# Performance work log

Hardware: AMD Instinct MI355X
Metric: run time of the kernel (lower is better)

The kernel has to match this reference:

```python
import jax, jax.numpy as jnp
import numpy as np


def _dct1d_last(x, W_r, W_i):
    """DCT-II along last axis via the even/odd-reorder + FFT trick, ortho norm.

    x: [..., N] real. W_r/W_i: [1, N] rows = cos/sin(-k*pi/(2N)).
    """
    N = x.shape[-1]
    # v = [x[0], x[2], ...] ++ [x[N-1], x[N-3], ..., x[1]]  (torch index/inverted_index)
    v = jnp.concatenate([x[..., 0::2], x[..., 1::2][..., ::-1]], axis=-1)
    Vc = jnp.fft.fft(v, axis=-1)  # complex64
    V = Vc.real * W_r - Vc.imag * W_i  # [..., N]
    # ortho normalization: V[0] /= sqrt(N)*2 ; V[1:] /= sqrt(N/2)*2 ; then V *= 2
    s0 = 1.0 / (np.sqrt(N) * 2.0)
    s1 = 1.0 / (np.sqrt(N / 2.0) * 2.0)
    scale = jnp.concatenate([jnp.full((1,), s0, x.dtype), jnp.full((N - 1,), s1, x.dtype)])
    return 2.0 * V * scale


def setup_inputs() -> dict:
    key = jax.random.key(0)
    H, W = 512, 512
    x = jax.random.normal(key, (32, 3, H, W), dtype=jnp.float32)
    kw = -jnp.arange(W, dtype=jnp.float32)[None, :] * np.pi / (2 * W)
    kh = -jnp.arange(H, dtype=jnp.float32)[None, :] * np.pi / (2 * H)
    return {
        "x": x,
        "W_r_weight": jnp.cos(kw), "W_i_weight": jnp.sin(kw),
        "W_r_height": jnp.cos(kh), "W_i_height": jnp.sin(kh),
    }


def reference(x, W_r_weight, W_i_weight, W_r_height, W_i_height):
    # DCT along width (last axis)
    V = _dct1d_last(x, W_r_weight, W_i_weight)
    # transpose last two dims, DCT along height, transpose back
    V = jnp.swapaxes(V, -1, -2)
    V = _dct1d_last(V, W_r_height, W_i_height)
    return jnp.swapaxes(V, -1, -2)
```

## Files before the change

kernel.cpp:

```cpp
#include <hip/hip_runtime.h>
#include <math.h>

#define NN 512

typedef __attribute__((ext_vector_type(8))) short bf16x8;
typedef __attribute__((ext_vector_type(4))) float f32x4;
typedef __attribute__((ext_vector_type(4))) unsigned int u32x4;

__device__ inline unsigned short f2bf(float f) {
    unsigned u = __builtin_bit_cast(unsigned, f);
    u += 0x7fffu + ((u >> 16) & 1u);
    return (unsigned short)(u >> 16);
}
__device__ inline float bf2f(unsigned short h) {
    unsigned u = ((unsigned)h) << 16;
    return __builtin_bit_cast(float, u);
}
__device__ inline unsigned cvtpk_bf16(float lo, float hi) {
    unsigned r;
    asm("v_cvt_pk_bf16_f32 %0, %1, %2" : "=v"(r) : "v"(lo), "v"(hi));
    return r;
}

__global__ __launch_bounds__(256) void fill_dct_half(unsigned short* __restrict__ Ce,
                                                     unsigned short* __restrict__ Co) {
    int idx = blockIdx.x * 256 + threadIdx.x;
    int par = idx >> 16;
    int kk = (idx >> 8) & 255;
    int n = idx & 255;
    int k = 2 * kk + par;
    int m = ((2 * n + 1) * k) & 2047;
    float ang = (float)m * 3.0679615757712823e-3f;
    float s = (k == 0) ? 0.04419417382415922f : 0.0625f;
    unsigned short v = f2bf(s * cosf(ang));
    if (par) Co[kk * 256 + n] = v; else Ce[kk * 256 + n] = v;
}

#define GLB(p) ((const __attribute__((address_space(1))) unsigned int*)(const void*)(p))
#define LDS(p) ((__attribute__((address_space(3))) unsigned int*)(p))

template <int PASS>
__global__ __launch_bounds__(256, 3) void gemm_dct(const void* __restrict__ Ap,
                                                   const unsigned short* __restrict__ Ce,
                                                   const unsigned short* __restrict__ Cop,
                                                   void* __restrict__ Outp,
                                                   size_t strideIn, size_t strideOut) {
    const int nwg = (int)gridDim.x;
    const int cpx = nwg >> 3;
    const int bid = (int)blockIdx.x;
    const int nid = (bid & 7) * cpx + (bid >> 3);
    const int bx = nid & 3;
    const int by = (nid >> 2) & 3;
    const int bz = nid >> 4;

    __shared__ unsigned short sm[24576];
    unsigned short* As = sm;
    unsigned short* Bs = sm + 12288;

    const int t = threadIdx.x;
    const int lane = t & 63;
    const int wave = t >> 6;
    const int wr = wave >> 1, wc = wave & 1;
    const int lr = lane & 15;
    const int kgx = ((lane >> 4) * 8) ^ (((lr >> 1) & 3) << 3);

    const int srow = t >> 2;
    const int sslot = t & 3;
    const int scol = (sslot ^ ((srow >> 1) & 3)) * 8;

    const int frow = t >> 1;
    const int fhalf = t & 1;
    const int fs0 = fhalf * 2;
    const int fxw = (frow >> 1) & 3;
    const int fslot0 = (fs0 ^ fxw) * 8;
    const int fslot1 = ((fs0 + 1) ^ fxw) * 8;

    const float* Xf = nullptr;
    const unsigned short* Tp = nullptr;
    const unsigned short* Gmat;
    int grow0, sgn, row0, col0;
    if constexpr (PASS == 1) {
        Xf = (const float*)Ap + (size_t)bz * strideIn;
        row0 = by * 128;
        col0 = bx * 128;
        Gmat = (bx < 2) ? Ce : Cop; grow0 = (bx & 1) * 128; sgn = (bx >= 2);
    } else {
        Tp = (const unsigned short*)Ap + (size_t)bz * strideIn;
        col0 = bx * 128;
        row0 = 0;
        Gmat = (by < 2) ? Ce : Cop; grow0 = (by & 1) * 128; sgn = (by >= 2);
    }
    const float sgnf = sgn ? -1.0f : 1.0f;

    f32x4 acc[4][4] = {};

    f32x4 rf[4], rm[4];
    bf16x8 gf[2], gm[2];

    auto stageG = [&](unsigned short* dst, int buf, int k0) {
        __builtin_amdgcn_global_load_lds(GLB(Gmat + (size_t)(grow0 + srow) * 256 + k0 + scol),
                                         LDS(&dst[buf * 4096 + srow * 32 + sslot * 8]), 16, 0, 0);
        __builtin_amdgcn_global_load_lds(GLB(Gmat + (size_t)(grow0 + 64 + srow) * 256 + k0 + scol),
                                         LDS(&dst[buf * 4096 + (64 + srow) * 32 + sslot * 8]), 16, 0, 0);
    };
    auto loadRaw1 = [&](int k0) {
        const float* bfp = Xf + (size_t)(row0 + frow) * NN + k0 + fhalf * 16;
        const float* bmp = Xf + (size_t)(row0 + frow) * NN + (496 - k0 - fhalf * 16);
#pragma unroll
        for (int q = 0; q < 4; ++q) {
            rf[q] = *reinterpret_cast<const f32x4*>(bfp + 4 * q);
            rm[q] = *reinterpret_cast<const f32x4*>(bmp + 4 * q);
        }
    };
    auto combineWrite1 = [&](int buf) {
        unsigned p[8];
#pragma unroll
        for (int q = 0; q < 8; ++q) {
            const int j0 = 2 * q, j1 = 2 * q + 1;
            const int r0 = 15 - j0, r1 = 15 - j1;
            float s0 = fmaf(sgnf, rm[r0 >> 2][r0 & 3], rf[j0 >> 2][j0 & 3]);
            float s1 = fmaf(sgnf, rm[r1 >> 2][r1 & 3], rf[j1 >> 2][j1 & 3]);
            p[q] = cvtpk_bf16(s0, s1);
        }
        u32x4 w0 = {p[0], p[1], p[2], p[3]};
        u32x4 w1 = {p[4], p[5], p[6], p[7]};
        *reinterpret_cast<u32x4*>(&As[buf * 4096 + frow * 32 + fslot0]) = w0;
        *reinterpret_cast<u32x4*>(&As[buf * 4096 + frow * 32 + fslot1]) = w1;
    };
    auto loadRaw2 = [&](int k0) {
        const unsigned short* bfp = Tp + (size_t)(col0 + frow) * NN + k0 + fhalf * 16;
        const unsigned short* bmp = Tp + (size_t)(col0 + frow) * NN + (496 - k0 - fhalf * 16);
        gf[0] = *reinterpret_cast<const bf16x8*>(bfp);
        gf[1] = *reinterpret_cast<const bf16x8*>(bfp + 8);
        gm[0] = *reinterpret_cast<const bf16x8*>(bmp);
        gm[1] = *reinterpret_cast<const bf16x8*>(bmp + 8);
    };
    auto combineWrite2 = [&](int buf) {
        unsigned p[8];
#pragma unroll
        for (int q = 0; q < 8; ++q) {
            const int j0 = 2 * q, j1 = 2 * q + 1;
            const int r0 = 15 - j0, r1 = 15 - j1;
            float a0 = bf2f((unsigned short)gf[j0 >> 3][j0 & 7]);
            float a1 = bf2f((unsigned short)gf[j1 >> 3][j1 & 7]);
            float b0 = bf2f((unsigned short)gm[r0 >> 3][r0 & 7]);
            float b1 = bf2f((unsigned short)gm[r1 >> 3][r1 & 7]);
            p[q] = cvtpk_bf16(fmaf(sgnf, b0, a0), fmaf(sgnf, b1, a1));
        }
        u32x4 w0 = {p[0], p[1], p[2], p[3]};
        u32x4 w1 = {p[4], p[5], p[6], p[7]};
        *reinterpret_cast<u32x4*>(&Bs[buf * 4096 + frow * 32 + fslot0]) = w0;
        *reinterpret_cast<u32x4*>(&Bs[buf * 4096 + frow * 32 + fslot1]) = w1;
    };
    auto compute = [&](int buf) {
        bf16x8 a[4], b[4];
#pragma unroll
        for (int mi = 0; mi < 4; ++mi)
            a[mi] = *reinterpret_cast<const bf16x8*>(
                &As[buf * 4096 + (wr * 64 + mi * 16 + lr) * 32 + kgx]);
#pragma unroll
        for (int ni = 0; ni < 4; ++ni)
            b[ni] = *reinterpret_cast<const bf16x8*>(
                &Bs[buf * 4096 + (wc * 64 + ni * 16 + lr) * 32 + kgx]);
        __builtin_amdgcn_s_setprio(1);
#pragma unroll
        for (int mi = 0; mi < 4; ++mi)
#pragma unroll
            for (int ni = 0; ni < 4; ++ni)
                acc[mi][ni] = __builtin_amdgcn_mfma_f32_16x16x32_bf16(a[mi], b[ni],
                                                                      acc[mi][ni], 0, 0, 0);
        __builtin_amdgcn_s_setprio(0);
    };

    if constexpr (PASS == 1) {
        stageG(Bs, 0, 0);  loadRaw1(0);
        asm volatile("" ::: "memory");
        combineWrite1(0);
        stageG(Bs, 1, 32); loadRaw1(32);
        asm volatile("s_waitcnt lgkmcnt(0)" ::: "memory");
        asm volatile("s_waitcnt vmcnt(10)" ::: "memory");
        __builtin_amdgcn_s_barrier();
    } else {
        stageG(As, 0, 0);  loadRaw2(0);
        asm volatile("" ::: "memory");
        combineWrite2(0);
        stageG(As, 1, 32); loadRaw2(32);
        asm volatile("s_waitcnt lgkmcnt(0)" ::: "memory");
        asm volatile("s_waitcnt vmcnt(6)" ::: "memory");
        __builtin_amdgcn_s_barrier();
    }

#pragma unroll
    for (int kt = 0; kt < 8; ++kt) {
        if (kt + 1 <= 7) {
            if constexpr (PASS == 1) combineWrite1((kt + 1) % 3);
            else                     combineWrite2((kt + 1) % 3);
        }
        if (kt + 2 <= 7) {
            if constexpr (PASS == 1) { stageG(Bs, (kt + 2) % 3, (kt + 2) * 32); loadRaw1((kt + 2) * 32); }
            else                     { stageG(As, (kt + 2) % 3, (kt + 2) * 32); loadRaw2((kt + 2) * 32); }
        }
        compute(kt % 3);
        asm volatile("s_waitcnt lgkmcnt(0)" ::: "memory");
        if (kt <= 5) {
            if constexpr (PASS == 1) asm volatile("s_waitcnt vmcnt(10)" ::: "memory");
            else                     asm volatile("s_waitcnt vmcnt(6)" ::: "memory");
        } else if (kt == 6) {
            asm volatile("s_waitcnt vmcnt(0)" ::: "memory");
        }
        if (kt < 7) __builtin_amdgcn_s_barrier();
    }

    if constexpr (PASS == 1) {
        unsigned short* T = (unsigned short*)Outp + (size_t)bz * strideOut;
        __syncthreads();
#pragma unroll
        for (int mi = 0; mi < 4; ++mi)
#pragma unroll
            for (int ni = 0; ni < 4; ++ni) {
                int gr = wr * 64 + mi * 16 + (lane >> 4) * 4;
                int gc = wc * 64 + ni * 16 + lr;
                ushort4 v;
                v.x = f2bf(acc[mi][ni][0]);
                v.y = f2bf(acc[mi][ni][1]);
                v.z = f2bf(acc[mi][ni][2]);
                v.w = f2bf(acc[mi][ni][3]);
                *reinterpret_cast<ushort4*>(&sm[gc * 132 + gr]) = v;
            }
        __syncthreads();
#pragma unroll
        for (int it = 0; it < 8; ++it) {
            int gcr = wave * 32 + it * 4 + (lane >> 4);
            int physRow = (bx & 1) * 256 + 2 * gcr + (bx >> 1);
            int cb = lr * 8;
            u32x4 d = *reinterpret_cast<const u32x4*>(&sm[gcr * 132 + cb]);
            *reinterpret_cast<u32x4*>(&T[(size_t)physRow * NN + row0 + cb]) = d;
        }
    } else {
        float* O = (float*)Outp + (size_t)bz * strideOut;
#pragma unroll
        for (int mi = 0; mi < 4; ++mi)
#pragma unroll
            for (int ni = 0; ni < 4; ++ni) {
                int gc = col0 + wc * 64 + ni * 16 + lr;
#pragma unroll
                for (int rr = 0; rr < 4; ++rr) {
                    int grl = wr * 64 + mi * 16 + (lane >> 4) * 4 + rr;
                    int ih = (by & 1) * 128 + grl;
                    int q = 2 * ih + (by >> 1);
                    O[(size_t)q * NN + gc] = acc[mi][ni][rr];
                }
            }
    }
}

extern "C" void kernel_launch(void* const* d_in, const int* in_sizes, int n_in,
                              void* d_out, int out_size, void* d_ws, size_t ws_size,
                              hipStream_t stream) {
    const float* x = (const float*)d_in[0];
    float* out = (float*)d_out;

    const int imgs = in_sizes[0] / (NN * NN);
    const size_t imgElems = (size_t)NN * NN;
    const size_t imgB16 = imgElems * 2;

    unsigned short* Ce = (unsigned short*)d_ws;
    unsigned short* Co = Ce + 65536;
    unsigned short* Tb = Co + 65536;

    long long budget = (long long)ws_size - 262144;
    int maxchunk = (int)(budget / (long long)imgB16);
    if (maxchunk < 1) maxchunk = 1;
    if (maxchunk > imgs) maxchunk = imgs;

    hipLaunchKernelGGL(fill_dct_half, dim3(512), dim3(256), 0, stream, Ce, Co);

    for (int i0 = 0; i0 < imgs; i0 += maxchunk) {
        int c = imgs - i0 < maxchunk ? imgs - i0 : maxchunk;
        hipLaunchKernelGGL((gemm_dct<1>), dim3(16 * c), dim3(256), 0, stream,
                           x + (size_t)i0 * imgElems, Ce, Co, Tb, imgElems, imgElems);
        hipLaunchKernelGGL((gemm_dct<2>), dim3(16 * c), dim3(256), 0, stream,
                           Tb, Ce, Co, out + (size_t)i0 * imgElems, imgElems, imgElems);
    }
}
```

Before: 78.05 us.

## Deepen register prefetch to three stages and shrink LDS for higher occupancy

The raw-operand global loads are now issued three k-steps ahead using two alternating register sets, and the combined operand is written into a double-buffered LDS tile rather than a triple-buffered one, while the weight tile staged through global_load_lds keeps three buffers. This cuts shared memory per block, and launch bounds are raised from 3 to 4 blocks per CU to hide more global-load latency. The cost is extra register pressure from the duplicated prefetch registers under a tighter register budget, which could cause spills, and the vmcnt wait counts had to be retuned by hand.

New measurement: 270.7 us. 247% more time.

```diff
diff --git a/kernel.cpp b/kernel.cpp
--- a/kernel.cpp
+++ b/kernel.cpp
@@ -40,7 +40,7 @@
 #define LDS(p) ((__attribute__((address_space(3))) unsigned int*)(p))
 
 template <int PASS>
-__global__ __launch_bounds__(256, 3) void gemm_dct(const void* __restrict__ Ap,
+__global__ __launch_bounds__(256, 4) void gemm_dct(const void* __restrict__ Ap,
                                                    const unsigned short* __restrict__ Ce,
                                                    const unsigned short* __restrict__ Cop,
                                                    void* __restrict__ Outp,
@@ -53,9 +53,9 @@
     const int by = (nid >> 2) & 3;
     const int bz = nid >> 4;
 
-    __shared__ unsigned short sm[24576];
-    unsigned short* As = sm;
-    unsigned short* Bs = sm + 12288;
+    __shared__ unsigned short sm[20480];
+    unsigned short* const As = sm;
+    unsigned short* const Bs = sm + (PASS == 1 ? 8192 : 12288);
 
     const int t = threadIdx.x;
     const int lane = t & 63;
@@ -94,8 +94,8 @@
 
     f32x4 acc[4][4] = {};
 
-    f32x4 rf[4], rm[4];
-    bf16x8 gf[2], gm[2];
+    f32x4 rf0[4], rm0[4], rf1[4], rm1[4];
+    bf16x8 gf0[2], gm0[2], gf1[2], gm1[2];
 
     auto stageG = [&](unsigned short* dst, int buf, int k0) {
         __builtin_amdgcn_global_load_lds(GLB(Gmat + (size_t)(grow0 + srow) * 256 + k0 + scol),
@@ -103,7 +103,7 @@
         __builtin_amdgcn_global_load_lds(GLB(Gmat + (size_t)(grow0 + 64 + srow) * 256 + k0 + scol),
                                          LDS(&dst[buf * 4096 + (64 + srow) * 32 + sslot * 8]), 16, 0, 0);
     };
-    auto loadRaw1 = [&](int k0) {
+    auto lr1 = [&](f32x4 (&rf)[4], f32x4 (&rm)[4], int k0) {
         const float* bfp = Xf + (size_t)(row0 + frow) * NN + k0 + fhalf * 16;
         const float* bmp = Xf + (size_t)(row0 + frow) * NN + (496 - k0 - fhalf * 16);
 #pragma unroll
@@ -112,7 +112,7 @@
             rm[q] = *reinterpret_cast<const f32x4*>(bmp + 4 * q);
         }
     };
-    auto combineWrite1 = [&](int buf) {
+    auto cw1 = [&](f32x4 (&rf)[4], f32x4 (&rm)[4], int buf) {
         unsigned p[8];
 #pragma unroll
         for (int q = 0; q < 8; ++q) {
@@ -127,7 +127,7 @@
         *reinterpret_cast<u32x4*>(&As[buf * 4096 + frow * 32 + fslot0]) = w0;
         *reinterpret_cast<u32x4*>(&As[buf * 4096 + frow * 32 + fslot1]) = w1;
     };
-    auto loadRaw2 = [&](int k0) {
+    auto lr2 = [&](bf16x8 (&gf)[2], bf16x8 (&gm)[2], int k0) {
         const unsigned short* bfp = Tp + (size_t)(col0 + frow) * NN + k0 + fhalf * 16;
         const unsigned short* bmp = Tp + (size_t)(col0 + frow) * NN + (496 - k0 - fhalf * 16);
         gf[0] = *reinterpret_cast<const bf16x8*>(bfp);
@@ -135,7 +135,7 @@
         gm[0] = *reinterpret_cast<const bf16x8*>(bmp);
         gm[1] = *reinterpret_cast<const bf16x8*>(bmp + 8);
     };
-    auto combineWrite2 = [&](int buf) {
+    auto cw2 = [&](bf16x8 (&gf)[2], bf16x8 (&gm)[2], int buf) {
         unsigned p[8];
 #pragma unroll
         for (int q = 0; q < 8; ++q) {
@@ -152,16 +152,18 @@
         *reinterpret_cast<u32x4*>(&Bs[buf * 4096 + frow * 32 + fslot0]) = w0;
         *reinterpret_cast<u32x4*>(&Bs[buf * 4096 + frow * 32 + fslot1]) = w1;
     };
-    auto compute = [&](int buf) {
+    auto compute = [&](int kt) {
+        const int bA = (PASS == 1) ? (kt & 1) : (kt % 3);
+        const int bB = (PASS == 1) ? (kt % 3) : (kt & 1);
         bf16x8 a[4], b[4];
 #pragma unroll
         for (int mi = 0; mi < 4; ++mi)
             a[mi] = *reinterpret_cast<const bf16x8*>(
-                &As[buf * 4096 + (wr * 64 + mi * 16 + lr) * 32 + kgx]);
+                &As[bA * 4096 + (wr * 64 + mi * 16 + lr) * 32 + kgx]);
 #pragma unroll
         for (int ni = 0; ni < 4; ++ni)
             b[ni] = *reinterpret_cast<const bf16x8*>(
-                &Bs[buf * 4096 + (wc * 64 + ni * 16 + lr) * 32 + kgx]);
+                &Bs[bB * 4096 + (wc * 64 + ni * 16 + lr) * 32 + kgx]);
         __builtin_amdgcn_s_setprio(1);
 #pragma unroll
         for (int mi = 0; mi < 4; ++mi)
@@ -173,36 +175,56 @@
     };
 
     if constexpr (PASS == 1) {
-        stageG(Bs, 0, 0);  loadRaw1(0);
-        asm volatile("" ::: "memory");
-        combineWrite1(0);
-        stageG(Bs, 1, 32); loadRaw1(32);
+        stageG(Bs, 0, 0);
+        lr1(rf0, rm0, 0);
+        asm volatile("" ::: "memory");
+        cw1(rf0, rm0, 0);
+        stageG(Bs, 1, 32);
+        asm volatile("" ::: "memory");
+        lr1(rf1, rm1, 32);
+        lr1(rf0, rm0, 64);
+        asm volatile("s_waitcnt lgkmcnt(0)" ::: "memory");
+        asm volatile("s_waitcnt vmcnt(18)" ::: "memory");
+        __builtin_amdgcn_s_barrier();
+    } else {
+        stageG(As, 0, 0);
+        lr2(gf0, gm0, 0);
+        asm volatile("" ::: "memory");
+        cw2(gf0, gm0, 0);
+        stageG(As, 1, 32);
+        asm volatile("" ::: "memory");
+        lr2(gf1, gm1, 32);
+        lr2(gf0, gm0, 64);
         asm volatile("s_waitcnt lgkmcnt(0)" ::: "memory");
         asm volatile("s_waitcnt vmcnt(10)" ::: "memory");
         __builtin_amdgcn_s_barrier();
-    } else {
-        stageG(As, 0, 0);  loadRaw2(0);
-        asm volatile("" ::: "memory");
-        combineWrite2(0);
-        stageG(As, 1, 32); loadRaw2(32);
-        asm volatile("s_waitcnt lgkmcnt(0)" ::: "memory");
-        asm volatile("s_waitcnt vmcnt(6)" ::: "memory");
-        __builtin_amdgcn_s_barrier();
     }
 
 #pragma unroll
     for (int kt = 0; kt < 8; ++kt) {
         if (kt + 1 <= 7) {
-            if constexpr (PASS == 1) combineWrite1((kt + 1) % 3);
-            else                     combineWrite2((kt + 1) % 3);
-        }
-        if (kt + 2 <= 7) {
-            if constexpr (PASS == 1) { stageG(Bs, (kt + 2) % 3, (kt + 2) * 32); loadRaw1((kt + 2) * 32); }
-            else                     { stageG(As, (kt + 2) % 3, (kt + 2) * 32); loadRaw2((kt + 2) * 32); }
-        }
-        compute(kt % 3);
+            if constexpr (PASS == 1) {
+                if ((kt + 1) & 1) cw1(rf1, rm1, 1); else cw1(rf0, rm0, 0);
+            } else {
+                if ((kt + 1) & 1) cw2(gf1, gm1, 1); else cw2(gf0, gm0, 0);
+            }
+        }
+        if (kt + 2 <= 7)
+            stageG(PASS == 1 ? Bs : As, (kt + 2) % 3, (kt + 2) * 32);
+        asm volatile("" ::: "memory");
+        if (kt + 3 <= 7) {
+            if constexpr (PASS == 1) {
+                if ((kt + 3) & 1) lr1(rf1, rm1, (kt + 3) * 32); else lr1(rf0, rm0, (kt + 3) * 32);
+            } else {
+                if ((kt + 3) & 1) lr2(gf1, gm1, (kt + 3) * 32); else lr2(gf0, gm0, (kt + 3) * 32);
+            }
+        }
+        compute(kt);
         asm volatile("s_waitcnt lgkmcnt(0)" ::: "memory");
-        if (kt <= 5) {
+        if (kt <= 4) {
+            if constexpr (PASS == 1) asm volatile("s_waitcnt vmcnt(18)" ::: "memory");
+            else                     asm volatile("s_waitcnt vmcnt(10)" ::: "memory");
+        } else if (kt == 5) {
             if constexpr (PASS == 1) asm volatile("s_waitcnt vmcnt(10)" ::: "memory");
             else                     asm volatile("s_waitcnt vmcnt(6)" ::: "memory");
         } else if (kt == 6) {
```

## Use 512-thread blocks with 8 waves and deeper register prefetch pipeline

Applied to the files above, without the earlier changes.

Workgroups grow from 4 to 8 waves, so each wave computes a 64x32 tile instead of 64x64 and each thread loads half as much raw input per K-step. The raw-input path is restructured into a three-stage register pipeline (two register sets, double-buffered LDS), while the DCT-matrix tiles stay triple-buffered through global_load_lds. The epilogue uses a separate LDS region so the pass-1 transpose no longer needs an extra barrier. This aims for more latency hiding and occupancy, at the cost of larger LDS per block, more barrier participants and finely hand-tuned vmcnt counts.

Result: faster. 74.77 us (-4.2%).

```diff
diff --git a/kernel.cpp b/kernel.cpp
--- a/kernel.cpp
+++ b/kernel.cpp
@@ -40,7 +40,7 @@
 #define LDS(p) ((__attribute__((address_space(3))) unsigned int*)(p))
 
 template <int PASS>
-__global__ __launch_bounds__(256, 3) void gemm_dct(const void* __restrict__ Ap,
+__global__ __launch_bounds__(512, 4) void gemm_dct(const void* __restrict__ Ap,
                                                    const unsigned short* __restrict__ Ce,
                                                    const unsigned short* __restrict__ Cop,
                                                    void* __restrict__ Outp,
@@ -53,14 +53,17 @@
     const int by = (nid >> 2) & 3;
     const int bz = nid >> 4;
 
-    __shared__ unsigned short sm[24576];
-    unsigned short* As = sm;
-    unsigned short* Bs = sm + 12288;
+    __shared__ unsigned short sm[PASS == 1 ? 37376 : 20480];
+    unsigned short* const As = sm;
+    unsigned short* const Bs = sm + (PASS == 1 ? 8192 : 12288);
+    unsigned short* const Rs = (PASS == 1) ? As : Bs;
+    unsigned short* const Gs = (PASS == 1) ? Bs : As;
+    unsigned short* const smE = sm + 20480;
 
     const int t = threadIdx.x;
     const int lane = t & 63;
     const int wave = t >> 6;
-    const int wr = wave >> 1, wc = wave & 1;
+    const int wr = wave >> 2, wc = wave & 3;
     const int lr = lane & 15;
     const int kgx = ((lane >> 4) * 8) ^ (((lr >> 1) & 3) << 3);
 
@@ -68,12 +71,9 @@
     const int sslot = t & 3;
     const int scol = (sslot ^ ((srow >> 1) & 3)) * 8;
 
-    const int frow = t >> 1;
-    const int fhalf = t & 1;
-    const int fs0 = fhalf * 2;
-    const int fxw = (frow >> 1) & 3;
-    const int fslot0 = (fs0 ^ fxw) * 8;
-    const int fslot1 = ((fs0 + 1) ^ fxw) * 8;
+    const int frow = t >> 2;
+    const int fq = t & 3;
+    const int fslot = (fq ^ ((frow >> 1) & 3)) * 8;
 
     const float* Xf = nullptr;
     const unsigned short* Tp = nullptr;
@@ -92,119 +92,122 @@
     }
     const float sgnf = sgn ? -1.0f : 1.0f;
 
-    f32x4 acc[4][4] = {};
-
-    f32x4 rf[4], rm[4];
-    bf16x8 gf[2], gm[2];
-
-    auto stageG = [&](unsigned short* dst, int buf, int k0) {
+    f32x4 acc[4][2] = {};
+
+    f32x4 rfA[2], rmA[2], rfB[2], rmB[2];
+    bf16x8 gfA, gmA, gfB, gmB;
+
+    auto stageG = [&](int buf, int k0) {
         __builtin_amdgcn_global_load_lds(GLB(Gmat + (size_t)(grow0 + srow) * 256 + k0 + scol),
-                                         LDS(&dst[buf * 4096 + srow * 32 + sslot * 8]), 16, 0, 0);
-        __builtin_amdgcn_global_load_lds(GLB(Gmat + (size_t)(grow0 + 64 + srow) * 256 + k0 + scol),
-                                         LDS(&dst[buf * 4096 + (64 + srow) * 32 + sslot * 8]), 16, 0, 0);
-    };
-    auto loadRaw1 = [&](int k0) {
-        const float* bfp = Xf + (size_t)(row0 + frow) * NN + k0 + fhalf * 16;
-        const float* bmp = Xf + (size_t)(row0 + frow) * NN + (496 - k0 - fhalf * 16);
+                                         LDS(&Gs[buf * 4096 + srow * 32 + sslot * 8]), 16, 0, 0);
+    };
+    auto lr1 = [&](f32x4 (&rf)[2], f32x4 (&rm)[2], int k0) {
+        const float* bfp = Xf + (size_t)(row0 + frow) * NN + k0 + fq * 8;
+        const float* bmp = Xf + (size_t)(row0 + frow) * NN + (504 - k0 - fq * 8);
+        rf[0] = *reinterpret_cast<const f32x4*>(bfp);
+        rf[1] = *reinterpret_cast<const f32x4*>(bfp + 4);
+        rm[0] = *reinterpret_cast<const f32x4*>(bmp);
+        rm[1] = *reinterpret_cast<const f32x4*>(bmp + 4);
+    };
+    auto cw1 = [&](f32x4 (&rf)[2], f32x4 (&rm)[2], int buf) {
+        unsigned p[4];
 #pragma unroll
         for (int q = 0; q < 4; ++q) {
-            rf[q] = *reinterpret_cast<const f32x4*>(bfp + 4 * q);
-            rm[q] = *reinterpret_cast<const f32x4*>(bmp + 4 * q);
-        }
-    };
-    auto combineWrite1 = [&](int buf) {
-        unsigned p[8];
-#pragma unroll
-        for (int q = 0; q < 8; ++q) {
             const int j0 = 2 * q, j1 = 2 * q + 1;
-            const int r0 = 15 - j0, r1 = 15 - j1;
+            const int r0 = 7 - j0, r1 = 7 - j1;
             float s0 = fmaf(sgnf, rm[r0 >> 2][r0 & 3], rf[j0 >> 2][j0 & 3]);
             float s1 = fmaf(sgnf, rm[r1 >> 2][r1 & 3], rf[j1 >> 2][j1 & 3]);
             p[q] = cvtpk_bf16(s0, s1);
         }
-        u32x4 w0 = {p[0], p[1], p[2], p[3]};
-        u32x4 w1 = {p[4], p[5], p[6], p[7]};
-        *reinterpret_cast<u32x4*>(&As[buf * 4096 + frow * 32 + fslot0]) = w0;
-        *reinterpret_cast<u32x4*>(&As[buf * 4096 + frow * 32 + fslot1]) = w1;
-    };
-    auto loadRaw2 = [&](int k0) {
-        const unsigned short* bfp = Tp + (size_t)(col0 + frow) * NN + k0 + fhalf * 16;
-        const unsigned short* bmp = Tp + (size_t)(col0 + frow) * NN + (496 - k0 - fhalf * 16);
-        gf[0] = *reinterpret_cast<const bf16x8*>(bfp);
-        gf[1] = *reinterpret_cast<const bf16x8*>(bfp + 8);
-        gm[0] = *reinterpret_cast<const bf16x8*>(bmp);
-        gm[1] = *reinterpret_cast<const bf16x8*>(bmp + 8);
-    };
-    auto combineWrite2 = [&](int buf) {
-        unsigned p[8];
-#pragma unroll
-        for (int q = 0; q < 8; ++q) {
+        u32x4 w = {p[0], p[1], p[2], p[3]};
+        *reinterpret_cast<u32x4*>(&Rs[buf * 4096 + frow * 32 + fslot]) = w;
+    };
+    auto lr2 = [&](bf16x8& gf, bf16x8& gm, int k0) {
+        const unsigned short* bfp = Tp + (size_t)(col0 + frow) * NN + k0 + fq * 8;
+        const unsigned short* bmp = Tp + (size_t)(col0 + frow) * NN + (504 - k0 - fq * 8);
+        gf = *reinterpret_cast<const bf16x8*>(bfp);
+        gm = *reinterpret_cast<const bf16x8*>(bmp);
+    };
+    auto cw2 = [&](bf16x8& gf, bf16x8& gm, int buf) {
+        unsigned p[4];
+#pragma unroll
+        for (int q = 0; q < 4; ++q) {
             const int j0 = 2 * q, j1 = 2 * q + 1;
-            const int r0 = 15 - j0, r1 = 15 - j1;
-            float a0 = bf2f((unsigned short)gf[j0 >> 3][j0 & 7]);
-            float a1 = bf2f((unsigned short)gf[j1 >> 3][j1 & 7]);
-            float b0 = bf2f((unsigned short)gm[r0 >> 3][r0 & 7]);
-            float b1 = bf2f((unsigned short)gm[r1 >> 3][r1 & 7]);
+            float a0 = bf2f((unsigned short)gf[j0]);
+            float a1 = bf2f((unsigned short)gf[j1]);
+            float b0 = bf2f((unsigned short)gm[7 - j0]);
+            float b1 = bf2f((unsigned short)gm[7 - j1]);
             p[q] = cvtpk_bf16(fmaf(sgnf, b0, a0), fmaf(sgnf, b1, a1));
         }
-        u32x4 w0 = {p[0], p[1], p[2], p[3]};
-        u32x4 w1 = {p[4], p[5], p[6], p[7]};
-        *reinterpret_cast<u32x4*>(&Bs[buf * 4096 + frow * 32 + fslot0]) = w0;
-        *reinterpret_cast<u32x4*>(&Bs[buf * 4096 + frow * 32 + fslot1]) = w1;
-    };
-    auto compute = [&](int buf) {
-        bf16x8 a[4], b[4];
+        u32x4 w = {p[0], p[1], p[2], p[3]};
+        *reinterpret_cast<u32x4*>(&Rs[buf * 4096 + frow * 32 + fslot]) = w;
+    };
+    auto compute = [&](int kt) {
+        const int rofs = (kt & 1) * 4096;
+        const int gofs = (kt % 3) * 4096;
+        const int aofs = (PASS == 1) ? rofs : gofs;
+        const int bofs = (PASS == 1) ? gofs : rofs;
+        bf16x8 a[4], b[2];
 #pragma unroll
         for (int mi = 0; mi < 4; ++mi)
             a[mi] = *reinterpret_cast<const bf16x8*>(
-                &As[buf * 4096 + (wr * 64 + mi * 16 + lr) * 32 + kgx]);
-#pragma unroll
-        for (int ni = 0; ni < 4; ++ni)
+                &As[aofs + (wr * 64 + mi * 16 + lr) * 32 + kgx]);
+#pragma unroll
+        for (int ni = 0; ni < 2; ++ni)
             b[ni] = *reinterpret_cast<const bf16x8*>(
-                &Bs[buf * 4096 + (wc * 64 + ni * 16 + lr) * 32 + kgx]);
+                &Bs[bofs + (wc * 32 + ni * 16 + lr) * 32 + kgx]);
         __builtin_amdgcn_s_setprio(1);
 #pragma unroll
         for (int mi = 0; mi < 4; ++mi)
 #pragma unroll
-            for (int ni = 0; ni < 4; ++ni)
+            for (int ni = 0; ni < 2; ++ni)
                 acc[mi][ni] = __builtin_amdgcn_mfma_f32_16x16x32_bf16(a[mi], b[ni],
                                                                       acc[mi][ni], 0, 0, 0);
         __builtin_amdgcn_s_setprio(0);
     };
-
-    if constexpr (PASS == 1) {
-        stageG(Bs, 0, 0);  loadRaw1(0);
+    auto doLR = [&](int s, int k0) {
+        if constexpr (PASS == 1) {
+            if (s & 1) lr1(rfB, rmB, k0); else lr1(rfA, rmA, k0);
+        } else {
+            if (s & 1) lr2(gfB, gmB, k0); else lr2(gfA, gmA, k0);
+        }
+    };
+    auto doCW = [&](int s) {
+        const int buf = s & 1;
+        if constexpr (PASS == 1) {
+            if (s & 1) cw1(rfB, rmB, buf); else cw1(rfA, rmA, buf);
+        } else {
+            if (s & 1) cw2(gfB, gmB, buf); else cw2(gfA, gmA, buf);
+        }
+    };
+
+    stageG(0, 0);
+    doLR(0, 0);
+    asm volatile("" ::: "memory");
+    doCW(0);
+    stageG(1, 32);
+    asm volatile("" ::: "memory");
+    doLR(1, 32);
+    doLR(2, 64);
+    asm volatile("s_waitcnt lgkmcnt(0)" ::: "memory");
+    if constexpr (PASS == 1) asm volatile("s_waitcnt vmcnt(8)" ::: "memory");
+    else                     asm volatile("s_waitcnt vmcnt(4)" ::: "memory");
+    __builtin_amdgcn_s_barrier();
+
+#pragma unroll
+    for (int kt = 0; kt < 8; ++kt) {
+        if (kt + 1 <= 7) doCW(kt + 1);
+        if (kt + 2 <= 7) stageG((kt + 2) % 3, (kt + 2) * 32);
         asm volatile("" ::: "memory");
-        combineWrite1(0);
-        stageG(Bs, 1, 32); loadRaw1(32);
+        if (kt + 3 <= 7) doLR(kt + 3, (kt + 3) * 32);
+        compute(kt);
         asm volatile("s_waitcnt lgkmcnt(0)" ::: "memory");
-        asm volatile("s_waitcnt vmcnt(10)" ::: "memory");
-        __builtin_amdgcn_s_barrier();
-    } else {
-        stageG(As, 0, 0);  loadRaw2(0);
-        asm volatile("" ::: "memory");
-        combineWrite2(0);
-        stageG(As, 1, 32); loadRaw2(32);
-        asm volatile("s_waitcnt lgkmcnt(0)" ::: "memory");
-        asm volatile("s_waitcnt vmcnt(6)" ::: "memory");
-        __builtin_amdgcn_s_barrier();
-    }
-
-#pragma unroll
-    for (int kt = 0; kt < 8; ++kt) {
-        if (kt + 1 <= 7) {
-            if constexpr (PASS == 1) combineWrite1((kt + 1) % 3);
-            else                     combineWrite2((kt + 1) % 3);
-        }
-        if (kt + 2 <= 7) {
-            if constexpr (PASS == 1) { stageG(Bs, (kt + 2) % 3, (kt + 2) * 32); loadRaw1((kt + 2) * 32); }
-            else                     { stageG(As, (kt + 2) % 3, (kt + 2) * 32); loadRaw2((kt + 2) * 32); }
-        }
-        compute(kt % 3);
-        asm volatile("s_waitcnt lgkmcnt(0)" ::: "memory");
-        if (kt <= 5) {
-            if constexpr (PASS == 1) asm volatile("s_waitcnt vmcnt(10)" ::: "memory");
-            else                     asm volatile("s_waitcnt vmcnt(6)" ::: "memory");
+        if (kt <= 4) {
+            if constexpr (PASS == 1) asm volatile("s_waitcnt vmcnt(9)" ::: "memory");
+            else                     asm volatile("s_waitcnt vmcnt(5)" ::: "memory");
+        } else if (kt == 5) {
+            if constexpr (PASS == 1) asm volatile("s_waitcnt vmcnt(5)" ::: "memory");
+            else                     asm volatile("s_waitcnt vmcnt(3)" ::: "memory");
         } else if (kt == 6) {
             asm volatile("s_waitcnt vmcnt(0)" ::: "memory");
         }
@@ -213,27 +216,27 @@
 
     if constexpr (PASS == 1) {
         unsigned short* T = (unsigned short*)Outp + (size_t)bz * strideOut;
-        __syncthreads();
-#pragma unroll
-        for (int mi = 0; mi < 4; ++mi)
-#pragma unroll
-            for (int ni = 0; ni < 4; ++ni) {
+#pragma unroll
+        for (int mi = 0; mi < 4; ++mi)
+#pragma unroll
+            for (int ni = 0; ni < 2; ++ni) {
                 int gr = wr * 64 + mi * 16 + (lane >> 4) * 4;
-                int gc = wc * 64 + ni * 16 + lr;
+                int gc = wc * 32 + ni * 16 + lr;
                 ushort4 v;
                 v.x = f2bf(acc[mi][ni][0]);
                 v.y = f2bf(acc[mi][ni][1]);
                 v.z = f2bf(acc[mi][ni][2]);
                 v.w = f2bf(acc[mi][ni][3]);
-                *reinterpret_cast<ushort4*>(&sm[gc * 132 + gr]) = v;
+                *reinterpret_cast<ushort4*>(&smE[gc * 132 + gr]) = v;
             }
-        __syncthreads();
-#pragma unroll
-        for (int it = 0; it < 8; ++it) {
-            int gcr = wave * 32 + it * 4 + (lane >> 4);
+        asm volatile("s_waitcnt lgkmcnt(0)" ::: "memory");
+        __builtin_amdgcn_s_barrier();
+#pragma unroll
+        for (int it = 0; it < 4; ++it) {
+            int gcr = wave * 16 + it * 4 + (lane >> 4);
             int physRow = (bx & 1) * 256 + 2 * gcr + (bx >> 1);
             int cb = lr * 8;
-            u32x4 d = *reinterpret_cast<const u32x4*>(&sm[gcr * 132 + cb]);
+            u32x4 d = *reinterpret_cast<const u32x4*>(&smE[gcr * 132 + cb]);
             *reinterpret_cast<u32x4*>(&T[(size_t)physRow * NN + row0 + cb]) = d;
         }
     } else {
@@ -241,8 +244,8 @@
 #pragma unroll
         for (int mi = 0; mi < 4; ++mi)
 #pragma unroll
-            for (int ni = 0; ni < 4; ++ni) {
-                int gc = col0 + wc * 64 + ni * 16 + lr;
+            for (int ni = 0; ni < 2; ++ni) {
+                int gc = col0 + wc * 32 + ni * 16 + lr;
 #pragma unroll
                 for (int rr = 0; rr < 4; ++rr) {
                     int grl = wr * 64 + mi * 16 + (lane >> 4) * 4 + rr;
@@ -277,9 +280,9 @@
 
     for (int i0 = 0; i0 < imgs; i0 += maxchunk) {
         int c = imgs - i0 < maxchunk ? imgs - i0 : maxchunk;
-        hipLaunchKernelGGL((gemm_dct<1>), dim3(16 * c), dim3(256), 0, stream,
+        hipLaunchKernelGGL((gemm_dct<1>), dim3(16 * c), dim3(512), 0, stream,
                            x + (size_t)i0 * imgElems, Ce, Co, Tb, imgElems, imgElems);
-        hipLaunchKernelGGL((gemm_dct<2>), dim3(16 * c), dim3(256), 0, stream,
+        hipLaunchKernelGGL((gemm_dct<2>), dim3(16 * c), dim3(512), 0, stream,
                            Tb, Ce, Co, out + (size_t)i0 * imgElems, imgElems, imgElems);
     }
 }
```

## Load data operand straight into MFMA fragments and widen blocks to 512 threads

Applied to the files above, without the earlier changes.

The input (pass 1) or intermediate (pass 2) operand, with its mirrored fold, is now read from global memory directly into registers in the MFMA fragment layout. It is combined in registers, so the LDS staging buffer and write for that operand are gone. Only the DCT half-matrix is still staged through LDS with async global-to-LDS loads. Blocks grow to 8 waves, each computing a 32x64 sub-tile, which cuts accumulator registers per wave and lowers LDS use. The trade-offs are less coalesced global reads per lane, and the explicit vmcnt waits are removed, so ordering of the async LDS loads depends on compiler-inserted waits.

After: 201.2 us. 2.58x slower.

```diff
diff --git a/kernel.cpp b/kernel.cpp
--- a/kernel.cpp
+++ b/kernel.cpp
@@ -40,7 +40,7 @@
 #define LDS(p) ((__attribute__((address_space(3))) unsigned int*)(p))
 
 template <int PASS>
-__global__ __launch_bounds__(256, 3) void gemm_dct(const void* __restrict__ Ap,
+__global__ __launch_bounds__(512, 4) void gemm_dct(const void* __restrict__ Ap,
                                                    const unsigned short* __restrict__ Ce,
                                                    const unsigned short* __restrict__ Cop,
                                                    void* __restrict__ Outp,
@@ -53,27 +53,21 @@
     const int by = (nid >> 2) & 3;
     const int bz = nid >> 4;
 
-    __shared__ unsigned short sm[24576];
-    unsigned short* As = sm;
-    unsigned short* Bs = sm + 12288;
+    __shared__ unsigned short sm[PASS == 1 ? 16896 : 12288];
+    unsigned short* const Gs = sm;
 
     const int t = threadIdx.x;
     const int lane = t & 63;
     const int wave = t >> 6;
-    const int wr = wave >> 1, wc = wave & 1;
+    const int wr = wave >> 1;
+    const int wc = wave & 1;
     const int lr = lane & 15;
-    const int kgx = ((lane >> 4) * 8) ^ (((lr >> 1) & 3) << 3);
+    const int oct = lane >> 4;
+    const int kgx = (oct * 8) ^ (((lr >> 1) & 3) << 3);
 
     const int srow = t >> 2;
     const int sslot = t & 3;
     const int scol = (sslot ^ ((srow >> 1) & 3)) * 8;
-
-    const int frow = t >> 1;
-    const int fhalf = t & 1;
-    const int fs0 = fhalf * 2;
-    const int fxw = (frow >> 1) & 3;
-    const int fslot0 = (fs0 ^ fxw) * 8;
-    const int fslot1 = ((fs0 + 1) ^ fxw) * 8;
 
     const float* Xf = nullptr;
     const unsigned short* Tp = nullptr;
@@ -92,133 +86,126 @@
     }
     const float sgnf = sgn ? -1.0f : 1.0f;
 
-    f32x4 acc[4][4] = {};
-
-    f32x4 rf[4], rm[4];
-    bf16x8 gf[2], gm[2];
-
-    auto stageG = [&](unsigned short* dst, int buf, int k0) {
+    f32x4 acc[2][4] = {};
+
+    f32x4 xf[2][2], xm[2][2];
+    bf16x8 tf[4], tm[4];
+
+    auto stageG = [&](int buf, int k0) {
         __builtin_amdgcn_global_load_lds(GLB(Gmat + (size_t)(grow0 + srow) * 256 + k0 + scol),
-                                         LDS(&dst[buf * 4096 + srow * 32 + sslot * 8]), 16, 0, 0);
-        __builtin_amdgcn_global_load_lds(GLB(Gmat + (size_t)(grow0 + 64 + srow) * 256 + k0 + scol),
-                                         LDS(&dst[buf * 4096 + (64 + srow) * 32 + sslot * 8]), 16, 0, 0);
+                                         LDS(&Gs[buf * 4096 + srow * 32 + sslot * 8]), 16, 0, 0);
     };
-    auto loadRaw1 = [&](int k0) {
-        const float* bfp = Xf + (size_t)(row0 + frow) * NN + k0 + fhalf * 16;
-        const float* bmp = Xf + (size_t)(row0 + frow) * NN + (496 - k0 - fhalf * 16);
-#pragma unroll
-        for (int q = 0; q < 4; ++q) {
-            rf[q] = *reinterpret_cast<const f32x4*>(bfp + 4 * q);
-            rm[q] = *reinterpret_cast<const f32x4*>(bmp + 4 * q);
+    auto loadRaw = [&](int k0) {
+        if constexpr (PASS == 1) {
+#pragma unroll
+            for (int mi = 0; mi < 2; ++mi) {
+                const float* rp = Xf + (size_t)(row0 + wr * 32 + mi * 16 + lr) * NN;
+                const float* fp = rp + k0 + oct * 8;
+                const float* mp = rp + (504 - k0 - oct * 8);
+                xf[mi][0] = *reinterpret_cast<const f32x4*>(fp);
+                xf[mi][1] = *reinterpret_cast<const f32x4*>(fp + 4);
+                xm[mi][0] = *reinterpret_cast<const f32x4*>(mp);
+                xm[mi][1] = *reinterpret_cast<const f32x4*>(mp + 4);
+            }
+        } else {
+#pragma unroll
+            for (int ni = 0; ni < 4; ++ni) {
+                const unsigned short* rp = Tp + (size_t)(col0 + wc * 64 + ni * 16 + lr) * NN;
+                tf[ni] = *reinterpret_cast<const bf16x8*>(rp + k0 + oct * 8);
+                tm[ni] = *reinterpret_cast<const bf16x8*>(rp + (504 - k0 - oct * 8));
+            }
         }
     };
-    auto combineWrite1 = [&](int buf) {
-        unsigned p[8];
-#pragma unroll
-        for (int q = 0; q < 8; ++q) {
-            const int j0 = 2 * q, j1 = 2 * q + 1;
-            const int r0 = 15 - j0, r1 = 15 - j1;
-            float s0 = fmaf(sgnf, rm[r0 >> 2][r0 & 3], rf[j0 >> 2][j0 & 3]);
-            float s1 = fmaf(sgnf, rm[r1 >> 2][r1 & 3], rf[j1 >> 2][j1 & 3]);
-            p[q] = cvtpk_bf16(s0, s1);
-        }
-        u32x4 w0 = {p[0], p[1], p[2], p[3]};
-        u32x4 w1 = {p[4], p[5], p[6], p[7]};
-        *reinterpret_cast<u32x4*>(&As[buf * 4096 + frow * 32 + fslot0]) = w0;
-        *reinterpret_cast<u32x4*>(&As[buf * 4096 + frow * 32 + fslot1]) = w1;
-    };
-    auto loadRaw2 = [&](int k0) {
-        const unsigned short* bfp = Tp + (size_t)(col0 + frow) * NN + k0 + fhalf * 16;
-        const unsigned short* bmp = Tp + (size_t)(col0 + frow) * NN + (496 - k0 - fhalf * 16);
-        gf[0] = *reinterpret_cast<const bf16x8*>(bfp);
-        gf[1] = *reinterpret_cast<const bf16x8*>(bfp + 8);
-        gm[0] = *reinterpret_cast<const bf16x8*>(bmp);
-        gm[1] = *reinterpret_cast<const bf16x8*>(bmp + 8);
-    };
-    auto combineWrite2 = [&](int buf) {
-        unsigned p[8];
-#pragma unroll
-        for (int q = 0; q < 8; ++q) {
-            const int j0 = 2 * q, j1 = 2 * q + 1;
-            const int r0 = 15 - j0, r1 = 15 - j1;
-            float a0 = bf2f((unsigned short)gf[j0 >> 3][j0 & 7]);
-            float a1 = bf2f((unsigned short)gf[j1 >> 3][j1 & 7]);
-            float b0 = bf2f((unsigned short)gm[r0 >> 3][r0 & 7]);
-            float b1 = bf2f((unsigned short)gm[r1 >> 3][r1 & 7]);
-            p[q] = cvtpk_bf16(fmaf(sgnf, b0, a0), fmaf(sgnf, b1, a1));
-        }
-        u32x4 w0 = {p[0], p[1], p[2], p[3]};
-        u32x4 w1 = {p[4], p[5], p[6], p[7]};
-        *reinterpret_cast<u32x4*>(&Bs[buf * 4096 + frow * 32 + fslot0]) = w0;
-        *reinterpret_cast<u32x4*>(&Bs[buf * 4096 + frow * 32 + fslot1]) = w1;
-    };
-    auto compute = [&](int buf) {
-        bf16x8 a[4], b[4];
-#pragma unroll
-        for (int mi = 0; mi < 4; ++mi)
-            a[mi] = *reinterpret_cast<const bf16x8*>(
-                &As[buf * 4096 + (wr * 64 + mi * 16 + lr) * 32 + kgx]);
-#pragma unroll
-        for (int ni = 0; ni < 4; ++ni)
-            b[ni] = *reinterpret_cast<const bf16x8*>(
-                &Bs[buf * 4096 + (wc * 64 + ni * 16 + lr) * 32 + kgx]);
+
+    auto step = [&](int kt, bool doStage, bool doLoad) {
+        const int gofs = (kt % 3) * 4096;
+        if (doStage) stageG((kt + 2) % 3, (kt + 2) * 32);
+        asm volatile("" ::: "memory");
+
+        bf16x8 fr[PASS == 1 ? 2 : 4];
+        if constexpr (PASS == 1) {
+#pragma unroll
+            for (int mi = 0; mi < 2; ++mi) {
+                float f[8];
+#pragma unroll
+                for (int j = 0; j < 8; ++j) {
+                    const int r = 7 - j;
+                    float w = xf[mi][j >> 2][j & 3];
+                    float m = xm[mi][r >> 2][r & 3];
+                    f[j] = fmaf(sgnf, m, w);
+                }
+                u32x4 pk = {cvtpk_bf16(f[0], f[1]), cvtpk_bf16(f[2], f[3]),
+                            cvtpk_bf16(f[4], f[5]), cvtpk_bf16(f[6], f[7])};
+                fr[mi] = __builtin_bit_cast(bf16x8, pk);
+            }
+        } else {
+#pragma unroll
+            for (int ni = 0; ni < 4; ++ni) {
+                float f[8];
+#pragma unroll
+                for (int j = 0; j < 8; ++j) {
+                    float w = bf2f((unsigned short)tf[ni][j]);
+                    float m = bf2f((unsigned short)tm[ni][7 - j]);
+                    f[j] = fmaf(sgnf, m, w);
+                }
+                u32x4 pk = {cvtpk_bf16(f[0], f[1]), cvtpk_bf16(f[2], f[3]),
+                            cvtpk_bf16(f[4], f[5]), cvtpk_bf16(f[6], f[7])};
+                fr[ni] = __builtin_bit_cast(bf16x8, pk);
+            }
+        }
+
+        if (doLoad) loadRaw((kt + 1) * 32);
+
         __builtin_amdgcn_s_setprio(1);
-#pragma unroll
-        for (int mi = 0; mi < 4; ++mi)
+        if constexpr (PASS == 1) {
+            bf16x8 b[4];
 #pragma unroll
             for (int ni = 0; ni < 4; ++ni)
-                acc[mi][ni] = __builtin_amdgcn_mfma_f32_16x16x32_bf16(a[mi], b[ni],
-                                                                      acc[mi][ni], 0, 0, 0);
+                b[ni] = *reinterpret_cast<const bf16x8*>(
+                    &Gs[gofs + (wc * 64 + ni * 16 + lr) * 32 + kgx]);
+#pragma unroll
+            for (int mi = 0; mi < 2; ++mi)
+#pragma unroll
+                for (int ni = 0; ni < 4; ++ni)
+                    acc[mi][ni] = __builtin_amdgcn_mfma_f32_16x16x32_bf16(fr[mi], b[ni],
+                                                                          acc[mi][ni], 0, 0, 0);
+        } else {
+            bf16x8 a[2];
+#pragma unroll
+            for (int mi = 0; mi < 2; ++mi)
+                a[mi] = *reinterpret_cast<const bf16x8*>(
+                    &Gs[gofs + (wr * 32 + mi * 16 + lr) * 32 + kgx]);
+#pragma unroll
+            for (int mi = 0; mi < 2; ++mi)
+#pragma unroll
+                for (int ni = 0; ni < 4; ++ni)
+                    acc[mi][ni] = __builtin_amdgcn_mfma_f32_16x16x32_bf16(a[mi], fr[ni],
+                                                                          acc[mi][ni], 0, 0, 0);
+        }
         __builtin_amdgcn_s_setprio(0);
     };
 
-    if constexpr (PASS == 1) {
-        stageG(Bs, 0, 0);  loadRaw1(0);
-        asm volatile("" ::: "memory");
-        combineWrite1(0);
-        stageG(Bs, 1, 32); loadRaw1(32);
-        asm volatile("s_waitcnt lgkmcnt(0)" ::: "memory");
-        asm volatile("s_waitcnt vmcnt(10)" ::: "memory");
-        __builtin_amdgcn_s_barrier();
-    } else {
-        stageG(As, 0, 0);  loadRaw2(0);
-        asm volatile("" ::: "memory");
-        combineWrite2(0);
-        stageG(As, 1, 32); loadRaw2(32);
-        asm volatile("s_waitcnt lgkmcnt(0)" ::: "memory");
-        asm volatile("s_waitcnt vmcnt(6)" ::: "memory");
-        __builtin_amdgcn_s_barrier();
-    }
+    stageG(0, 0);
+    stageG(1, 32);
+    asm volatile("" ::: "memory");
+    loadRaw(0);
+    asm volatile("s_waitcnt vmcnt(0)" ::: "memory");
+    __builtin_amdgcn_s_barrier();
 
 #pragma unroll
     for (int kt = 0; kt < 8; ++kt) {
-        if (kt + 1 <= 7) {
-            if constexpr (PASS == 1) combineWrite1((kt + 1) % 3);
-            else                     combineWrite2((kt + 1) % 3);
-        }
-        if (kt + 2 <= 7) {
-            if constexpr (PASS == 1) { stageG(Bs, (kt + 2) % 3, (kt + 2) * 32); loadRaw1((kt + 2) * 32); }
-            else                     { stageG(As, (kt + 2) % 3, (kt + 2) * 32); loadRaw2((kt + 2) * 32); }
-        }
-        compute(kt % 3);
-        asm volatile("s_waitcnt lgkmcnt(0)" ::: "memory");
-        if (kt <= 5) {
-            if constexpr (PASS == 1) asm volatile("s_waitcnt vmcnt(10)" ::: "memory");
-            else                     asm volatile("s_waitcnt vmcnt(6)" ::: "memory");
-        } else if (kt == 6) {
-            asm volatile("s_waitcnt vmcnt(0)" ::: "memory");
-        }
+        step(kt, kt + 2 <= 7, kt + 1 <= 7);
         if (kt < 7) __builtin_amdgcn_s_barrier();
     }
 
     if constexpr (PASS == 1) {
         unsigned short* T = (unsigned short*)Outp + (size_t)bz * strideOut;
-        __syncthreads();
-#pragma unroll
-        for (int mi = 0; mi < 4; ++mi)
-#pragma unroll
-            for (int ni = 0; ni < 4; ++ni) {
-                int gr = wr * 64 + mi * 16 + (lane >> 4) * 4;
+        __builtin_amdgcn_s_barrier();
+#pragma unroll
+        for (int mi = 0; mi < 2; ++mi)
+#pragma unroll
+            for (int ni = 0; ni < 4; ++ni) {
+                int gr = wr * 32 + mi * 16 + (lane >> 4) * 4;
                 int gc = wc * 64 + ni * 16 + lr;
                 ushort4 v;
                 v.x = f2bf(acc[mi][ni][0]);
@@ -227,25 +214,26 @@
                 v.w = f2bf(acc[mi][ni][3]);
                 *reinterpret_cast<ushort4*>(&sm[gc * 132 + gr]) = v;
             }
-        __syncthreads();
-#pragma unroll
-        for (int it = 0; it < 8; ++it) {
-            int gcr = wave * 32 + it * 4 + (lane >> 4);
+        asm volatile("s_waitcnt lgkmcnt(0)" ::: "memory");
+        __builtin_amdgcn_s_barrier();
+#pragma unroll
+        for (int it = 0; it < 4; ++it) {
+            int gcr = it * 32 + (t >> 4);
             int physRow = (bx & 1) * 256 + 2 * gcr + (bx >> 1);
-            int cb = lr * 8;
+            int cb = (t & 15) * 8;
             u32x4 d = *reinterpret_cast<const u32x4*>(&sm[gcr * 132 + cb]);
             *reinterpret_cast<u32x4*>(&T[(size_t)physRow * NN + row0 + cb]) = d;
         }
     } else {
         float* O = (float*)Outp + (size_t)bz * strideOut;
 #pragma unroll
-        for (int mi = 0; mi < 4; ++mi)
+        for (int mi = 0; mi < 2; ++mi)
 #pragma unroll
             for (int ni = 0; ni < 4; ++ni) {
                 int gc = col0 + wc * 64 + ni * 16 + lr;
 #pragma unroll
                 for (int rr = 0; rr < 4; ++rr) {
-                    int grl = wr * 64 + mi * 16 + (lane >> 4) * 4 + rr;
+                    int grl = wr * 32 + mi * 16 + (lane >> 4) * 4 + rr;
                     int ih = (by & 1) * 128 + grl;
                     int q = 2 * ih + (by >> 1);
                     O[(size_t)q * NN + gc] = acc[mi][ni][rr];
@@ -277,9 +265,9 @@
 
     for (int i0 = 0; i0 < imgs; i0 += maxchunk) {
         int c = imgs - i0 < maxchunk ? imgs - i0 : maxchunk;
-        hipLaunchKernelGGL((gemm_dct<1>), dim3(16 * c), dim3(256), 0, stream,
+        hipLaunchKernelGGL((gemm_dct<1>), dim3(16 * c), dim3(512), 0, stream,
                            x + (size_t)i0 * imgElems, Ce, Co, Tb, imgElems, imgElems);
-        hipLaunchKernelGGL((gemm_dct<2>), dim3(16 * c), dim3(256), 0, stream,
+        hipLaunchKernelGGL((gemm_dct<2>), dim3(16 * c), dim3(512), 0, stream,
                            Tb, Ce, Co, out + (size_t)i0 * imgElems, imgElems, imgElems);
     }
 }
```
